# Performance work log

Measured on AMD Instinct MI355X. Metric: run time of the kernel, lower is better.

The kernel has to match this reference:

```python
import jax, jax.numpy as jnp
import numpy as np

EMBED = 1024
HEADS = 16
DEPTH = EMBED // HEADS
FFN_DIM = 4096
EPS = 1e-9


def layer_norm(x, g, b):
    mu = jnp.mean(x, axis=-1, keepdims=True)
    var = jnp.mean(jnp.square(x - mu), axis=-1, keepdims=True)
    return (x - mu) * jax.lax.rsqrt(var + EPS) * g + b


def setup_inputs() -> dict:
    key = jax.random.key(0)
    ks = jax.random.split(key, 16)
    B, S = 2, 2048
    s_e = 1.0 / np.sqrt(EMBED)
    s_f = 1.0 / np.sqrt(FFN_DIM)
    return {
        "x": jax.random.normal(ks[0], (B, S, EMBED), dtype=jnp.float32),
        "mask": jnp.zeros((B, 1, 1, S), dtype=jnp.float32),
        "wq_w": jax.random.normal(ks[1], (EMBED, EMBED), dtype=jnp.float32) * s_e,
        "wq_b": jnp.zeros((EMBED,), dtype=jnp.float32),
        "wk_w": jax.random.normal(ks[2], (EMBED, EMBED), dtype=jnp.float32) * s_e,
        "wk_b": jnp.zeros((EMBED,), dtype=jnp.float32),
        "wv_w": jax.random.normal(ks[3], (EMBED, EMBED), dtype=jnp.float32) * s_e,
        "wv_b": jnp.zeros((EMBED,), dtype=jnp.float32),
        "wo_w": jax.random.normal(ks[4], (EMBED, EMBED), dtype=jnp.float32) * s_e,
        "wo_b": jnp.zeros((EMBED,), dtype=jnp.float32),
        "f1_w": jax.random.normal(ks[5], (EMBED, FFN_DIM), dtype=jnp.float32) * s_e,
        "f1_b": jnp.zeros((FFN_DIM,), dtype=jnp.float32),
        "f2_w": jax.random.normal(ks[6], (FFN_DIM, EMBED), dtype=jnp.float32) * s_f,
        "f2_b": jnp.zeros((EMBED,), dtype=jnp.float32),
        "ln1_g": jnp.ones((EMBED,), dtype=jnp.float32),
        "ln1_b": jnp.zeros((EMBED,), dtype=jnp.float32),
        "ln2_g": jnp.ones((EMBED,), dtype=jnp.float32),
        "ln2_b": jnp.zeros((EMBED,), dtype=jnp.float32),
    }


def reference(x, mask, wq_w, wq_b, wk_w, wk_b, wv_w, wv_b, wo_w, wo_b,
              f1_w, f1_b, f2_w, f2_b, ln1_g, ln1_b, ln2_g, ln2_b):
    B, S, E = x.shape

    def split_heads(t):  # (B,S,E) -> (B,H,S,D)
        return t.reshape(B, S, HEADS, DEPTH).transpose(0, 2, 1, 3)

    q = split_heads(x @ wq_w + wq_b)
    k = split_heads(x @ wk_w + wk_b)
    v = split_heads(x @ wv_w + wv_b)

    logits = jnp.einsum("bhqd,bhkd->bhqk", q, k) / jnp.sqrt(jnp.float32(DEPTH))
    logits = logits + mask * -1e12  # mask broadcast (B,1,1,S)
    attn = jax.nn.softmax(logits, axis=-1)
    out = jnp.einsum("bhqk,bhkd->bhqd", attn, v)
    out = out.transpose(0, 2, 1, 3).reshape(B, S, E)
    out = out @ wo_w + wo_b

    # dropout is identity (is_train=False)
    h = layer_norm(out + x, ln1_g, ln1_b)
    f = jax.nn.relu(h @ f1_w + f1_b) @ f2_w + f2_b
    return layer_norm(f + h, ln2_g, ln2_b)
```

## Files before the change

kernel.cpp:

```cpp
#include <hip/hip_runtime.h>
#include <hip/hip_bf16.h>
#include <stdint.h>

typedef __hip_bfloat16 bf16;
typedef __attribute__((ext_vector_type(8))) short short8;
typedef __attribute__((ext_vector_type(4))) short short4v;
typedef __attribute__((ext_vector_type(4))) float floatx4;

#define E_DIM 1024
#define S_LEN 2048
#define NB    2
#define NH    16
#define HD    64
#define FFN   4096
#define MTOT  4096

#define QSCALE 0.18033688011112042f
#define MSCALE -1.4426950408889634e12f

__device__ __forceinline__ void gl_lds16(const void* g, void* l) {
  __builtin_amdgcn_global_load_lds(
      (__attribute__((address_space(1))) void*)(g),
      (__attribute__((address_space(3))) void*)(l), 16, 0, 0);
}

#define VMW(N)  do { asm volatile("s_waitcnt vmcnt(" #N ")" ::: "memory"); \
                     __builtin_amdgcn_sched_barrier(0); } while (0)
#define LGKM0   do { asm volatile("s_waitcnt lgkmcnt(0)" ::: "memory"); } while (0)
#define BARR    do { asm volatile("s_barrier" ::: "memory"); } while (0)

__device__ __forceinline__ float exp2_fast(float x) {
  float r;
  asm("v_exp_f32 %0, %1" : "=v"(r) : "v"(x));
  return r;
}

__device__ __forceinline__ int fswz_v(int row) { return row & 7; }
__device__ __forceinline__ int fswz_k(int row) {
  return ((row ^ (row >> 3)) & 3) | ((((row >> 3) ^ (row >> 4)) & 1) << 2);
}

__device__ __forceinline__ float bf16bits2float(short s) {
  union { unsigned u; float f; } c;
  c.u = ((unsigned)(unsigned short)s) << 16;
  return c.f;
}

__global__ __launch_bounds__(256)
void cvt_bf16(const float* __restrict__ in, bf16* __restrict__ out) {
  const size_t i = ((size_t)blockIdx.x * 256 + threadIdx.x) * 4;
  float4 v = *(const float4*)(in + i);
  out[i + 0] = __float2bfloat16(v.x);
  out[i + 1] = __float2bfloat16(v.y);
  out[i + 2] = __float2bfloat16(v.z);
  out[i + 3] = __float2bfloat16(v.w);
}

__global__ __launch_bounds__(256)
void transpose_all(const float* __restrict__ wq, const float* __restrict__ wk,
                   const float* __restrict__ wv, const float* __restrict__ wo,
                   const float* __restrict__ f1, const float* __restrict__ f2,
                   bf16* __restrict__ W3T, bf16* __restrict__ woT,
                   bf16* __restrict__ f1T, bf16* __restrict__ f2T) {
  const int z = blockIdx.z;
  const float* in;
  bf16* out;
  int inStride, outStride, rOff, cOff;
  if (z < 4) {
    in = (z == 0) ? wq : (z == 1) ? wk : (z == 2) ? wv : wo;
    out = (z < 3) ? (W3T + (size_t)z * 1024 * 1024) : woT;
    inStride = 1024; outStride = 1024; rOff = 0; cOff = 0;
  } else if (z < 8) {
    in = f1; out = f1T; inStride = 4096; outStride = 1024;
    rOff = 0; cOff = (z - 4) * 1024;
  } else {
    in = f2; out = f2T; inStride = 1024; outStride = 4096;
    rOff = (z - 8) * 1024; cOff = 0;
  }
  __shared__ float tile[32][33];
  const int tx = threadIdx.x & 31;
  const int ty = threadIdx.x >> 5;
  const int c0 = blockIdx.x * 32;
  const int r0 = blockIdx.y * 32;
#pragma unroll
  for (int j = 0; j < 32; j += 8)
    tile[ty + j][tx] =
        in[(size_t)(rOff + r0 + ty + j) * inStride + cOff + c0 + tx];
  __syncthreads();
#pragma unroll
  for (int j = 0; j < 32; j += 8)
    out[(size_t)(cOff + c0 + ty + j) * outStride + rOff + r0 + tx] =
        __float2bfloat16(tile[tx][ty + j]);
}

__global__ __launch_bounds__(256)
void prep_bias(const float* __restrict__ qb, const float* __restrict__ kb,
               const float* __restrict__ vb, float* __restrict__ out) {
  const int i = blockIdx.x * 256 + threadIdx.x;
  float v = (i < 1024) ? qb[i] * QSCALE
                       : ((i < 2048) ? kb[i - 1024] : vb[i - 2048]);
  out[i] = v;
}

__global__ __launch_bounds__(512, 2)
void gemm256(const bf16* __restrict__ A, const bf16* __restrict__ B,
             const float* __restrict__ bias, void* __restrict__ Cout,
             void* __restrict__ Cout2,
             int M, int N, int Kpart, int lda, int mode) {
  __shared__ alignas(16) bf16 sA[2][2][128 * 64];
  __shared__ alignas(16) bf16 sB[2][2][128 * 64];
  const int tid   = threadIdx.x;
  const int wave  = tid >> 6;
  const int lane  = tid & 63;
  const int row16 = lane & 15;
  const int quad  = lane >> 4;
  const int sw7   = row16 & 7;

  const int gx = gridDim.x;
  const int nwg = gx * gridDim.y;
  const int cpx = nwg >> 3;
  int id = blockIdx.y * gx + blockIdx.x;
  id = (id & 7) * cpx + (id >> 3);
  const int m0 = (id % gx) * 256;
  const int n0 = (id / gx) * 256;

  const int wm2 = wave >> 2;
  const int wn4 = wave & 3;
  const int wm  = wm2 * 128;
  const int wn  = wn4 * 64;
  const int hB  = wn4 >> 1;
  const int rbB = (wn4 & 1) * 64;
  const int koff = blockIdx.z * Kpart;
  const int NS = Kpart >> 6;

  floatx4 acc[8][4];
#pragma unroll
  for (int i = 0; i < 8; i++)
#pragma unroll
    for (int j = 0; j < 4; j++) {
      floatx4 z = {0.f, 0.f, 0.f, 0.f};
      acc[i][j] = z;
    }

  auto stage_half = [&](const bf16* G, int rowBase, int k0, bf16* dst) {
#pragma unroll
    for (int j = 0; j < 2; ++j) {
      const int r = wave * 16 + j * 8 + (lane >> 3);
      const int g = (lane & 7) ^ (r & 7);
      gl_lds16(G + (size_t)(rowBase + r) * lda + k0 + g * 8,
               dst + (wave * 16 + j * 8) * 64);
    }
  };
  auto stage_tile = [&](int t, int p) {
    const int k0 = koff + t * 64;
    stage_half(A, m0,       k0, &sA[p][0][0]);
    stage_half(A, m0 + 128, k0, &sA[p][1][0]);
    stage_half(B, n0,       k0, &sB[p][0][0]);
    stage_half(B, n0 + 128, k0, &sB[p][1][0]);
  };

  short8 aF[8][2];
  short8 bF[4][2];
  const bf16* aH = nullptr;
  const bf16* bH = nullptr;

  auto read_aF = [&](int mi0) {
#pragma unroll
    for (int mi = 0; mi < 4; ++mi)
#pragma unroll
      for (int kk = 0; kk < 2; ++kk)
        aF[mi0 + mi][kk] = *(const short8*)(
            aH + ((mi0 + mi) * 16 + row16) * 64 + (((kk * 4 + quad) ^ sw7) << 3));
  };
  auto read_bF = [&](int ni0) {
#pragma unroll
    for (int ni = 0; ni < 2; ++ni)
#pragma unroll
      for (int kk = 0; kk < 2; ++kk)
        bF[ni0 + ni][kk] = *(const short8*)(
            bH + (rbB + (ni0 + ni) * 16 + row16) * 64 + (((kk * 4 + quad) ^ sw7) << 3));
  };
  auto qmf = [&](int mi0, int ni0) {
    __builtin_amdgcn_s_setprio(1);
#pragma unroll
    for (int mi = 0; mi < 4; ++mi)
#pragma unroll
      for (int ni = 0; ni < 2; ++ni)
#pragma unroll
        for (int kk = 0; kk < 2; ++kk)
          acc[mi0 + mi][ni0 + ni] = __builtin_amdgcn_mfma_f32_16x16x32_bf16(
              aF[mi0 + mi][kk], bF[ni0 + ni][kk], acc[mi0 + mi][ni0 + ni], 0, 0, 0);
    __builtin_amdgcn_s_setprio(0);
  };

  stage_tile(0, 0);
  stage_tile(1, 1);

  for (int s = 0; s < NS; ++s) {
    const int b = s & 1;
    aH = &sA[b][wm2][0];
    bH = &sB[b][hB][0];
    if (s + 1 < NS) VMW(8); else VMW(0);
    BARR;
    read_bF(0);
    read_bF(2);
    read_aF(0);
    qmf(0, 0);
    qmf(0, 2);
    read_aF(4);
    LGKM0;
    BARR;
    if (s + 2 < NS) stage_tile(s + 2, b);
    qmf(4, 0);
    qmf(4, 2);
  }

  float bval[4] = {0.f, 0.f, 0.f, 0.f};
  if (mode != 0) {
#pragma unroll
    for (int ni = 0; ni < 4; ni++) bval[ni] = bias[n0 + wn + ni * 16 + row16];
  }

#pragma unroll
  for (int mi = 0; mi < 8; mi++) {
#pragma unroll
    for (int ni = 0; ni < 4; ni++) {
      const int col = n0 + wn + ni * 16 + row16;
      if (mode == 0) {
        float* co = (float*)((blockIdx.z < 2) ? Cout : Cout2) +
                    (size_t)(blockIdx.z & 1) * M * N;
#pragma unroll
        for (int r = 0; r < 4; r++) {
          const int row = m0 + wm + mi * 16 + quad * 4 + r;
          co[(size_t)row * N + col] = acc[mi][ni][r];
        }
      } else if (mode == 1) {
#pragma unroll
        for (int r = 0; r < 4; r++) {
          const int row = m0 + wm + mi * 16 + quad * 4 + r;
          float v = acc[mi][ni][r] + bval[ni];
          v = v > 0.f ? v : 0.f;
          ((bf16*)Cout)[(size_t)row * N + col] = __float2bfloat16(v);
        }
      } else {
        const int mat = col >> 10;
        const int c10 = col & 1023;
        const int hh = c10 >> 6, dd = c10 & 63;
        const float scl = (mat == 0) ? QSCALE : 1.0f;
        bf16* qout = (bf16*)Cout;
        const int rbase = m0 + wm + mi * 16 + quad * 4;
        const int b2 = rbase >> 11, ss = rbase & 2047;
        const size_t bh = (size_t)b2 * NH + hh;
        if (mat == 2) {
          bf16* vt = qout + (1 << 23);
          short4v pv;
#pragma unroll
          for (int r = 0; r < 4; r++) {
            bf16 t = __float2bfloat16(acc[mi][ni][r] + bval[ni]);
            pv[r] = *(short*)&t;
          }
          *(short4v*)(vt + (bh * HD + dd) * S_LEN + ss) = pv;
        } else {
          bf16* o = (mat == 1) ? (qout + (1 << 22)) : qout;
#pragma unroll
          for (int r = 0; r < 4; r++) {
            float v = acc[mi][ni][r] * scl + bval[ni];
            o[(bh * S_LEN + ss + r) * HD + dd] = __float2bfloat16(v);
          }
        }
      }
    }
  }
}

__global__ __launch_bounds__(256, 4)
void flash_attn(const bf16* __restrict__ Q, const bf16* __restrict__ K,
                const bf16* __restrict__ Vt, const float* __restrict__ mask,
                bf16* __restrict__ Out) {
  __shared__ alignas(16) bf16 sK[2][64 * 64];
  __shared__ alignas(16) bf16 sV[2][64 * 64];
  __shared__ alignas(16) float sM[S_LEN];

  const int tid   = threadIdx.x;
  const int wave  = tid >> 6;
  const int lane  = tid & 63;
  const int row16 = lane & 15;
  const int quad  = lane >> 4;
  const int bh = blockIdx.y;
  const int b = bh >> 4, h = bh & 15;
  const int q0 = blockIdx.x * 64;
  const int qg = q0 + wave * 16 + row16;

  const bf16* qp = Q + ((size_t)bh * S_LEN + qg) * HD;
  short8 qf0 = *(const short8*)(qp + quad * 8);
  short8 qf1 = *(const short8*)(qp + 32 + quad * 8);

  for (int i = tid; i < S_LEN / 4; i += 256) {
    float4 mv = ((const float4*)(mask + (size_t)b * S_LEN))[i];
    float4 w = {MSCALE * mv.x, MSCALE * mv.y, MSCALE * mv.z, MSCALE * mv.w};
    ((float4*)sM)[i] = w;
  }
  LGKM0;

  short8 ones;
#pragma unroll
  for (int j = 0; j < 8; j++) ones[j] = (short)0x3F80;

  floatx4 lacc = {0.f, 0.f, 0.f, 0.f};
  floatx4 ov[4];
#pragma unroll
  for (int i = 0; i < 4; i++) { floatx4 z = {0.f,0.f,0.f,0.f}; ov[i] = z; }

  const bf16* Kbase = K + (size_t)bh * S_LEN * HD;
  const bf16* Vbase = Vt + (size_t)bh * HD * S_LEN;
  const int NT = S_LEN / 64;

  auto stage = [&](int kt) {
    const bf16* Kg = Kbase + (size_t)kt * 64 * HD;
    const bf16* Vg = Vbase + kt * 64;
    bf16* dK = sK[kt & 1];
    bf16* dV = sV[kt & 1];
#pragma unroll
    for (int j = 0; j < 2; ++j) {
      const int ch = wave * 2 + j;
      const int row = ch * 8 + (lane >> 3);
      const int sc_ = lane & 7;
      gl_lds16(Kg + row * 64 + ((sc_ ^ fswz_k(row)) * 8), dK + ch * 512);
      gl_lds16(Vg + (size_t)row * S_LEN + ((sc_ ^ fswz_v(row)) * 8), dV + ch * 512);
    }
  };

  stage(0);

  for (int kt = 0; kt < NT; ++kt) {
    if (kt + 1 < NT) {
      stage(kt + 1);
      VMW(4);
    } else {
      VMW(0);
    }
    BARR;

    const bf16* Kb = sK[kt & 1];
    const bf16* Vb = sV[kt & 1];

    floatx4 sc[4];
#pragma unroll
    for (int mi = 0; mi < 4; mi++) {
      const int row = ((row16 >> 2) << 3) + (row16 & 3) + ((mi & 1) << 2) + ((mi >> 1) << 5);
      const int fk = fswz_k(row);
      short8 kf0 = *(const short8*)(Kb + row * 64 + ((quad ^ fk) << 3));
      short8 kf1 = *(const short8*)(Kb + row * 64 + (((4 + quad) ^ fk) << 3));
      floatx4 z = {0.f, 0.f, 0.f, 0.f};
      z = __builtin_amdgcn_mfma_f32_16x16x32_bf16(kf0, qf0, z, 0, 0, 0);
      sc[mi] = __builtin_amdgcn_mfma_f32_16x16x32_bf16(kf1, qf1, z, 0, 0, 0);
    }

#pragma unroll
    for (int mi = 0; mi < 4; mi++) {
      float4 mv = *(const float4*)(sM + kt * 64 + (quad << 3) + ((mi & 1) << 2) + ((mi >> 1) << 5));
      sc[mi][0] = exp2_fast(sc[mi][0] + mv.x);
      sc[mi][1] = exp2_fast(sc[mi][1] + mv.y);
      sc[mi][2] = exp2_fast(sc[mi][2] + mv.z);
      sc[mi][3] = exp2_fast(sc[mi][3] + mv.w);
    }

    short8 pf[2];
#pragma unroll
    for (int ks = 0; ks < 2; ks++)
#pragma unroll
      for (int jp = 0; jp < 4; jp++) {
        const int mi = 2 * ks + (jp >> 1);
        const int r0 = (jp & 1) * 2;
        bf16 p0 = __float2bfloat16(sc[mi][r0]);
        bf16 p1 = __float2bfloat16(sc[mi][r0 + 1]);
        pf[ks][2 * jp]     = *(short*)&p0;
        pf[ks][2 * jp + 1] = *(short*)&p1;
      }

    lacc = __builtin_amdgcn_mfma_f32_16x16x32_bf16(ones, pf[0], lacc, 0, 0, 0);
    lacc = __builtin_amdgcn_mfma_f32_16x16x32_bf16(ones, pf[1], lacc, 0, 0, 0);

#pragma unroll
    for (int mi = 0; mi < 4; mi++) {
      const int row = mi * 16 + row16;
      const int fv = fswz_v(row);
      short8 v0 = *(const short8*)(Vb + row * 64 + ((quad ^ fv) << 3));
      short8 v1 = *(const short8*)(Vb + row * 64 + (((4 + quad) ^ fv) << 3));
      ov[mi] = __builtin_amdgcn_mfma_f32_16x16x32_bf16(v0, pf[0], ov[mi], 0, 0, 0);
      ov[mi] = __builtin_amdgcn_mfma_f32_16x16x32_bf16(v1, pf[1], ov[mi], 0, 0, 0);
    }
    BARR;
  }

  const float inv = 1.0f / lacc[0];
#pragma unroll
  for (int mi = 0; mi < 4; mi++) {
    short4v pv;
#pragma unroll
    for (int r = 0; r < 4; r++) {
      bf16 t = __float2bfloat16(ov[mi][r] * inv);
      pv[r] = *(short*)&t;
    }
    *(short4v*)(Out + ((size_t)(b * S_LEN + qg)) * E_DIM + h * HD + mi * 16 + quad * 4) = pv;
  }
}

__global__ __launch_bounds__(256)
void ln_reduce(const float* __restrict__ p0, const float* __restrict__ p1,
               const float* __restrict__ p2, const float* __restrict__ p3,
               const float* __restrict__ resf, const bf16* __restrict__ resb,
               const float* __restrict__ bias, const float* __restrict__ g,
               const float* __restrict__ be, float* __restrict__ outf,
               bf16* __restrict__ outb) {
  const int row = blockIdx.x;
  const int tid = threadIdx.x;
  const size_t base = (size_t)row * 1024;
  const int c = tid * 4;
  float4 a = *(const float4*)(p0 + base + c);
  float4 bq = *(const float4*)(p1 + base + c);
  float4 xv;
  xv.x = a.x + bq.x;
  xv.y = a.y + bq.y;
  xv.z = a.z + bq.z;
  xv.w = a.w + bq.w;
  if (p2) {
    float4 a2 = *(const float4*)(p2 + base + c);
    float4 a3 = *(const float4*)(p3 + base + c);
    xv.x += a2.x + a3.x;
    xv.y += a2.y + a3.y;
    xv.z += a2.z + a3.z;
    xv.w += a2.w + a3.w;
  }
  float4 rv;
  if (resf) {
    rv = *(const float4*)(resf + base + c);
  } else {
    short4v rb = *(const short4v*)((const short*)resb + base + c);
    rv.x = bf16bits2float(rb[0]);
    rv.y = bf16bits2float(rb[1]);
    rv.z = bf16bits2float(rb[2]);
    rv.w = bf16bits2float(rb[3]);
  }
  float4 bi = *(const float4*)(bias + c);
  xv.x += rv.x + bi.x;
  xv.y += rv.y + bi.y;
  xv.z += rv.z + bi.z;
  xv.w += rv.w + bi.w;
  float s  = xv.x + xv.y + xv.z + xv.w;
  float s2 = xv.x * xv.x + xv.y * xv.y + xv.z * xv.z + xv.w * xv.w;
#pragma unroll
  for (int d = 1; d < 64; d <<= 1) {
    s  += __shfl_xor(s, d);
    s2 += __shfl_xor(s2, d);
  }
  __shared__ float red[2][4];
  const int wave = tid >> 6;
  if ((tid & 63) == 0) { red[0][wave] = s; red[1][wave] = s2; }
  __syncthreads();
  s  = red[0][0] + red[0][1] + red[0][2] + red[0][3];
  s2 = red[1][0] + red[1][1] + red[1][2] + red[1][3];
  const float mu  = s * (1.0f / 1024.0f);
  const float var = s2 * (1.0f / 1024.0f) - mu * mu;
  const float rs  = rsqrtf(var + 1e-9f);
  float4 gg = *(const float4*)(g + c);
  float4 bb = *(const float4*)(be + c);
  float4 y;
  y.x = (xv.x - mu) * rs * gg.x + bb.x;
  y.y = (xv.y - mu) * rs * gg.y + bb.y;
  y.z = (xv.z - mu) * rs * gg.z + bb.z;
  y.w = (xv.w - mu) * rs * gg.w + bb.w;
  if (outf) *(float4*)(outf + base + c) = y;
  if (outb) {
    bf16* o = outb + base + c;
    o[0] = __float2bfloat16(y.x);
    o[1] = __float2bfloat16(y.y);
    o[2] = __float2bfloat16(y.z);
    o[3] = __float2bfloat16(y.w);
  }
}

extern "C" void kernel_launch(void* const* d_in, const int* in_sizes, int n_in,
                              void* d_out, int out_size, void* d_ws,
                              size_t ws_size, hipStream_t stream) {
  const float* x    = (const float*)d_in[0];
  const float* mask = (const float*)d_in[1];
  const float* wq_w = (const float*)d_in[2];
  const float* wq_b = (const float*)d_in[3];
  const float* wk_w = (const float*)d_in[4];
  const float* wk_b = (const float*)d_in[5];
  const float* wv_w = (const float*)d_in[6];
  const float* wv_b = (const float*)d_in[7];
  const float* wo_w = (const float*)d_in[8];
  const float* wo_b = (const float*)d_in[9];
  const float* f1_w = (const float*)d_in[10];
  const float* f1_b = (const float*)d_in[11];
  const float* f2_w = (const float*)d_in[12];
  const float* f2_b = (const float*)d_in[13];
  const float* ln1_g = (const float*)d_in[14];
  const float* ln1_b = (const float*)d_in[15];
  const float* ln2_g = (const float*)d_in[16];
  const float* ln2_b = (const float*)d_in[17];
  float* out = (float*)d_out;

  char* ws = (char*)d_ws;
  const size_t MB = 1u << 20;
  bf16*  xbf   = (bf16*)(ws + 0 * MB);
  bf16*  W3T   = (bf16*)(ws + 8 * MB);
  bf16*  woT   = (bf16*)(ws + 14 * MB);
  float* bqkv  = (float*)(ws + 16 * MB);
  bf16*  Qb    = (bf16*)(ws + 17 * MB);
  bf16*  attnb = (bf16*)(ws + 0 * MB);
  bf16*  ffn1  = (bf16*)(ws + 17 * MB);
  bf16*  f1T   = (bf16*)(ws + 49 * MB);
  bf16*  f2T   = (bf16*)(ws + 57 * MB);
  float* P01   = (float*)(ws + 65 * MB);
  bf16*  hbf   = (bf16*)(ws + 97 * MB);
  float* P23   = (float*)(ws + 105 * MB);
  const size_t PS = (size_t)MTOT * E_DIM;

  const int KS = (ws_size >= (size_t)137 * MB) ? 4 : 2;
  const float* p2 = (KS == 4) ? P23 : nullptr;
  const float* p3 = (KS == 4) ? P23 + PS : nullptr;

  cvt_bf16<<<4096, 256, 0, stream>>>(x, xbf);
  transpose_all<<<dim3(32, 32, 12), 256, 0, stream>>>(
      wq_w, wk_w, wv_w, wo_w, f1_w, f2_w, W3T, woT, f1T, f2T);
  prep_bias<<<12, 256, 0, stream>>>(wq_b, wk_b, wv_b, bqkv);

  gemm256<<<dim3(16, 12, 1), 512, 0, stream>>>(
      xbf, W3T, bqkv, Qb, nullptr, MTOT, 3 * E_DIM, E_DIM, E_DIM, 2);

  flash_attn<<<dim3(S_LEN / 64, NB * NH), 256, 0, stream>>>(
      Qb, Qb + (1 << 22), Qb + (1 << 23), mask, attnb);

  gemm256<<<dim3(16, 4, KS), 512, 0, stream>>>(
      attnb, woT, nullptr, P01, P23, MTOT, E_DIM, E_DIM / KS, E_DIM, 0);

  ln_reduce<<<MTOT, 256, 0, stream>>>(P01, P01 + PS, p2, p3, x, nullptr,
                                      wo_b, ln1_g, ln1_b, nullptr, hbf);

  gemm256<<<dim3(16, 16, 1), 512, 0, stream>>>(
      hbf, f1T, f1_b, ffn1, nullptr, MTOT, FFN, E_DIM, E_DIM, 1);

  gemm256<<<dim3(16, 4, KS), 512, 0, stream>>>(
      ffn1, f2T, nullptr, P01, P23, MTOT, E_DIM, FFN / KS, FFN, 0);

  ln_reduce<<<MTOT, 256, 0, stream>>>(P01, P01 + PS, p2, p3, nullptr, hbf,
                                      f2_b, ln2_g, ln2_b, out, nullptr);
}
```

Baseline: 358.8 us.

## Process two 16-row query tiles per wave in flash attention

Each wave now handles 32 query rows instead of 16, so every block covers 128 queries and the grid is halved. Each K/V fragment read from LDS is reused for two query tiles, which halves K/V global traffic and LDS reads per query. The cost is more registers per thread, so launch bounds drop from 4 to 2 blocks per CU, and there are fewer blocks (512) to fill the GPU.

```diff
diff --git a/kernel.cpp b/kernel.cpp
--- a/kernel.cpp
+++ b/kernel.cpp
@@ -273,7 +273,7 @@
   }
 }
 
-__global__ __launch_bounds__(256, 4)
+__global__ __launch_bounds__(256, 2)
 void flash_attn(const bf16* __restrict__ Q, const bf16* __restrict__ K,
                 const bf16* __restrict__ Vt, const float* __restrict__ mask,
                 bf16* __restrict__ Out) {
@@ -288,12 +288,15 @@
   const int quad  = lane >> 4;
   const int bh = blockIdx.y;
   const int b = bh >> 4, h = bh & 15;
-  const int q0 = blockIdx.x * 64;
-  const int qg = q0 + wave * 16 + row16;
-
-  const bf16* qp = Q + ((size_t)bh * S_LEN + qg) * HD;
-  short8 qf0 = *(const short8*)(qp + quad * 8);
-  short8 qf1 = *(const short8*)(qp + 32 + quad * 8);
+  const int q0 = blockIdx.x * 128;
+  const int qg = q0 + wave * 32 + row16;
+
+  const bf16* qpA = Q + ((size_t)bh * S_LEN + qg) * HD;
+  const bf16* qpB = qpA + 16 * HD;
+  short8 qa0 = *(const short8*)(qpA + quad * 8);
+  short8 qa1 = *(const short8*)(qpA + 32 + quad * 8);
+  short8 qb0 = *(const short8*)(qpB + quad * 8);
+  short8 qb1 = *(const short8*)(qpB + 32 + quad * 8);
 
   for (int i = tid; i < S_LEN / 4; i += 256) {
     float4 mv = ((const float4*)(mask + (size_t)b * S_LEN))[i];
@@ -306,10 +309,14 @@
 #pragma unroll
   for (int j = 0; j < 8; j++) ones[j] = (short)0x3F80;
 
-  floatx4 lacc = {0.f, 0.f, 0.f, 0.f};
-  floatx4 ov[4];
-#pragma unroll
-  for (int i = 0; i < 4; i++) { floatx4 z = {0.f,0.f,0.f,0.f}; ov[i] = z; }
+  floatx4 laccA = {0.f, 0.f, 0.f, 0.f};
+  floatx4 laccB = {0.f, 0.f, 0.f, 0.f};
+  floatx4 ovA[4], ovB[4];
+#pragma unroll
+  for (int i = 0; i < 4; i++) {
+    floatx4 z = {0.f,0.f,0.f,0.f};
+    ovA[i] = z; ovB[i] = z;
+  }
 
   const bf16* Kbase = K + (size_t)bh * S_LEN * HD;
   const bf16* Vbase = Vt + (size_t)bh * HD * S_LEN;
@@ -344,42 +351,55 @@
     const bf16* Kb = sK[kt & 1];
     const bf16* Vb = sV[kt & 1];
 
-    floatx4 sc[4];
+    floatx4 scA[4], scB[4];
 #pragma unroll
     for (int mi = 0; mi < 4; mi++) {
       const int row = ((row16 >> 2) << 3) + (row16 & 3) + ((mi & 1) << 2) + ((mi >> 1) << 5);
       const int fk = fswz_k(row);
       short8 kf0 = *(const short8*)(Kb + row * 64 + ((quad ^ fk) << 3));
       short8 kf1 = *(const short8*)(Kb + row * 64 + (((4 + quad) ^ fk) << 3));
-      floatx4 z = {0.f, 0.f, 0.f, 0.f};
-      z = __builtin_amdgcn_mfma_f32_16x16x32_bf16(kf0, qf0, z, 0, 0, 0);
-      sc[mi] = __builtin_amdgcn_mfma_f32_16x16x32_bf16(kf1, qf1, z, 0, 0, 0);
+      floatx4 zA = {0.f, 0.f, 0.f, 0.f};
+      zA = __builtin_amdgcn_mfma_f32_16x16x32_bf16(kf0, qa0, zA, 0, 0, 0);
+      scA[mi] = __builtin_amdgcn_mfma_f32_16x16x32_bf16(kf1, qa1, zA, 0, 0, 0);
+      floatx4 zB = {0.f, 0.f, 0.f, 0.f};
+      zB = __builtin_amdgcn_mfma_f32_16x16x32_bf16(kf0, qb0, zB, 0, 0, 0);
+      scB[mi] = __builtin_amdgcn_mfma_f32_16x16x32_bf16(kf1, qb1, zB, 0, 0, 0);
     }
 
 #pragma unroll
     for (int mi = 0; mi < 4; mi++) {
       float4 mv = *(const float4*)(sM + kt * 64 + (quad << 3) + ((mi & 1) << 2) + ((mi >> 1) << 5));
-      sc[mi][0] = exp2_fast(sc[mi][0] + mv.x);
-      sc[mi][1] = exp2_fast(sc[mi][1] + mv.y);
-      sc[mi][2] = exp2_fast(sc[mi][2] + mv.z);
-      sc[mi][3] = exp2_fast(sc[mi][3] + mv.w);
-    }
-
-    short8 pf[2];
+      scA[mi][0] = exp2_fast(scA[mi][0] + mv.x);
+      scA[mi][1] = exp2_fast(scA[mi][1] + mv.y);
+      scA[mi][2] = exp2_fast(scA[mi][2] + mv.z);
+      scA[mi][3] = exp2_fast(scA[mi][3] + mv.w);
+      scB[mi][0] = exp2_fast(scB[mi][0] + mv.x);
+      scB[mi][1] = exp2_fast(scB[mi][1] + mv.y);
+      scB[mi][2] = exp2_fast(scB[mi][2] + mv.z);
+      scB[mi][3] = exp2_fast(scB[mi][3] + mv.w);
+    }
+
+    short8 pfA[2], pfB[2];
 #pragma unroll
     for (int ks = 0; ks < 2; ks++)
 #pragma unroll
       for (int jp = 0; jp < 4; jp++) {
         const int mi = 2 * ks + (jp >> 1);
         const int r0 = (jp & 1) * 2;
-        bf16 p0 = __float2bfloat16(sc[mi][r0]);
-        bf16 p1 = __float2bfloat16(sc[mi][r0 + 1]);
-        pf[ks][2 * jp]     = *(short*)&p0;
-        pf[ks][2 * jp + 1] = *(short*)&p1;
+        bf16 a0 = __float2bfloat16(scA[mi][r0]);
+        bf16 a1 = __float2bfloat16(scA[mi][r0 + 1]);
+        pfA[ks][2 * jp]     = *(short*)&a0;
+        pfA[ks][2 * jp + 1] = *(short*)&a1;
+        bf16 b0 = __float2bfloat16(scB[mi][r0]);
+        bf16 b1 = __float2bfloat16(scB[mi][r0 + 1]);
+        pfB[ks][2 * jp]     = *(short*)&b0;
+        pfB[ks][2 * jp + 1] = *(short*)&b1;
       }
 
-    lacc = __builtin_amdgcn_mfma_f32_16x16x32_bf16(ones, pf[0], lacc, 0, 0, 0);
-    lacc = __builtin_amdgcn_mfma_f32_16x16x32_bf16(ones, pf[1], lacc, 0, 0, 0);
+    laccA = __builtin_amdgcn_mfma_f32_16x16x32_bf16(ones, pfA[0], laccA, 0, 0, 0);
+    laccA = __builtin_amdgcn_mfma_f32_16x16x32_bf16(ones, pfA[1], laccA, 0, 0, 0);
+    laccB = __builtin_amdgcn_mfma_f32_16x16x32_bf16(ones, pfB[0], laccB, 0, 0, 0);
+    laccB = __builtin_amdgcn_mfma_f32_16x16x32_bf16(ones, pfB[1], laccB, 0, 0, 0);
 
 #pragma unroll
     for (int mi = 0; mi < 4; mi++) {
@@ -387,22 +407,28 @@
       const int fv = fswz_v(row);
       short8 v0 = *(const short8*)(Vb + row * 64 + ((quad ^ fv) << 3));
       short8 v1 = *(const short8*)(Vb + row * 64 + (((4 + quad) ^ fv) << 3));
-      ov[mi] = __builtin_amdgcn_mfma_f32_16x16x32_bf16(v0, pf[0], ov[mi], 0, 0, 0);
-      ov[mi] = __builtin_amdgcn_mfma_f32_16x16x32_bf16(v1, pf[1], ov[mi], 0, 0, 0);
+      ovA[mi] = __builtin_amdgcn_mfma_f32_16x16x32_bf16(v0, pfA[0], ovA[mi], 0, 0, 0);
+      ovA[mi] = __builtin_amdgcn_mfma_f32_16x16x32_bf16(v1, pfA[1], ovA[mi], 0, 0, 0);
+      ovB[mi] = __builtin_amdgcn_mfma_f32_16x16x32_bf16(v0, pfB[0], ovB[mi], 0, 0, 0);
+      ovB[mi] = __builtin_amdgcn_mfma_f32_16x16x32_bf16(v1, pfB[1], ovB[mi], 0, 0, 0);
     }
     BARR;
   }
 
-  const float inv = 1.0f / lacc[0];
+  const float invA = 1.0f / laccA[0];
+  const float invB = 1.0f / laccB[0];
 #pragma unroll
   for (int mi = 0; mi < 4; mi++) {
-    short4v pv;
+    short4v pva, pvb;
 #pragma unroll
     for (int r = 0; r < 4; r++) {
-      bf16 t = __float2bfloat16(ov[mi][r] * inv);
-      pv[r] = *(short*)&t;
-    }
-    *(short4v*)(Out + ((size_t)(b * S_LEN + qg)) * E_DIM + h * HD + mi * 16 + quad * 4) = pv;
+      bf16 ta = __float2bfloat16(ovA[mi][r] * invA);
+      pva[r] = *(short*)&ta;
+      bf16 tb = __float2bfloat16(ovB[mi][r] * invB);
+      pvb[r] = *(short*)&tb;
+    }
+    *(short4v*)(Out + ((size_t)(b * S_LEN + qg)) * E_DIM + h * HD + mi * 16 + quad * 4) = pva;
+    *(short4v*)(Out + ((size_t)(b * S_LEN + qg + 16)) * E_DIM + h * HD + mi * 16 + quad * 4) = pvb;
   }
 }
 
@@ -531,7 +557,7 @@
   gemm256<<<dim3(16, 12, 1), 512, 0, stream>>>(
       xbf, W3T, bqkv, Qb, nullptr, MTOT, 3 * E_DIM, E_DIM, E_DIM, 2);
 
-  flash_attn<<<dim3(S_LEN / 64, NB * NH), 256, 0, stream>>>(
+  flash_attn<<<dim3(S_LEN / 128, NB * NH), 256, 0, stream>>>(
       Qb, Qb + (1 << 22), Qb + (1 << 23), mask, attnb);
 
   gemm256<<<dim3(16, 4, KS), 512, 0, stream>>>(
```

Result: no change. 356.0 us (-0.8%).
